# Kernel optimization log

Measured on AMD Instinct MI355X. Metric: run time of the kernel, lower is better.

The kernel has to match this reference:

```python
import jax, jax.numpy as jnp
import numpy as np

D_MODEL = 2048
D_FF = 2048  # must equal D_MODEL: original code computes h @ (A@B).T
RANK = 4
ALPHA = 1.0
SCALE = ALPHA / RANK
B_SZ, SEQ = 4, 4096


def setup_inputs() -> dict:
    key = jax.random.key(0)
    ks = jax.random.split(key, 7)
    s1 = 1.0 / np.sqrt(D_MODEL)
    s2 = 1.0 / np.sqrt(D_FF)
    return {
        "x": jax.random.normal(ks[0], (B_SZ, SEQ, D_MODEL), jnp.float32),
        "W1": jax.random.normal(ks[1], (D_FF, D_MODEL), jnp.float32) * s1,   # torch Linear: (out,in)
        "b1": jax.random.normal(ks[2], (D_FF,), jnp.float32) * 0.01,
        "W2": jax.random.normal(ks[3], (D_MODEL, D_FF), jnp.float32) * s2,
        "b2": jax.random.normal(ks[4], (D_MODEL,), jnp.float32) * 0.01,
        "A": jax.random.normal(ks[5], (D_FF, RANK), jnp.float32) * 0.02,
        "B_lora": jax.random.normal(ks[6], (RANK, D_MODEL), jnp.float32) * 0.02,
    }


def reference(x, W1, b1, W2, b2, A, B_lora):
    # h = act(ffn[0](x)); ffn[1] = GELU
    h = jax.nn.gelu(jnp.einsum('bsd,fd->bsf', x, W1) + b1)   # [B,S,D_FF]
    # out = ffn[2](h)
    out = jnp.einsum('bsf,of->bso', h, W2) + b2              # [B,S,D_MODEL]
    # delta = h @ (A @ B).T * scale  (faithful: materializes (D_FF,D_MODEL) then transposes)
    delta = h @ (A @ B_lora).T * SCALE                       # requires D_FF == D_MODEL
    return out + delta
```

## Files before the change

### kernel.cpp

```cpp
#include <hip/hip_runtime.h>

typedef unsigned short u16;
typedef __attribute__((ext_vector_type(8))) short s16x8;
typedef __attribute__((ext_vector_type(4))) float f32x4;

#define D 2048
#define LORA_SCALE 0.25f

__device__ __forceinline__ u16 f2bf(float f) {
  unsigned u = __float_as_uint(f);
  unsigned r = u + 0x7fffu + ((u >> 16) & 1u);
  return (u16)(r >> 16);
}
__device__ __forceinline__ float bf2f(u16 h) {
  return __uint_as_float(((unsigned)h) << 16);
}

__device__ __forceinline__ void gload_lds16(const u16* g, u16* l) {
  __builtin_amdgcn_global_load_lds((const __attribute__((address_space(1))) void*)g,
                                   (__attribute__((address_space(3))) void*)l,
                                   16, 0, 0);
}

__global__ void split_fp32(const float* __restrict__ in, u16* __restrict__ hi,
                           u16* __restrict__ lo, int n4) {
  int i = blockIdx.x * 256 + threadIdx.x;
  if (i >= n4) return;
  float4 v = ((const float4*)in)[i];
  ushort4 h, l;
  h.x = f2bf(v.x); l.x = f2bf(v.x - bf2f(h.x));
  h.y = f2bf(v.y); l.y = f2bf(v.y - bf2f(h.y));
  h.z = f2bf(v.z); l.z = f2bf(v.z - bf2f(h.z));
  h.w = f2bf(v.w); l.w = f2bf(v.w - bf2f(h.w));
  ((ushort4*)hi)[i] = h;
  ((ushort4*)lo)[i] = l;
}

__global__ void w2eff_split(const float* __restrict__ W2, const float* __restrict__ A,
                            const float* __restrict__ Bl, u16* __restrict__ hi,
                            u16* __restrict__ lo) {
  int idx = blockIdx.x * 256 + threadIdx.x;
  int o = idx >> 9;
  int fq = idx & 511;
  float4 w = ((const float4*)(W2 + o * D))[fq];
  float a0 = A[o * 4 + 0], a1 = A[o * 4 + 1], a2 = A[o * 4 + 2], a3 = A[o * 4 + 3];
  float4 r0 = ((const float4*)(Bl + 0 * D))[fq];
  float4 r1 = ((const float4*)(Bl + 1 * D))[fq];
  float4 r2 = ((const float4*)(Bl + 2 * D))[fq];
  float4 r3 = ((const float4*)(Bl + 3 * D))[fq];
  w.x += LORA_SCALE * (a0 * r0.x + a1 * r1.x + a2 * r2.x + a3 * r3.x);
  w.y += LORA_SCALE * (a0 * r0.y + a1 * r1.y + a2 * r2.y + a3 * r3.y);
  w.z += LORA_SCALE * (a0 * r0.z + a1 * r1.z + a2 * r2.z + a3 * r3.z);
  w.w += LORA_SCALE * (a0 * r0.w + a1 * r1.w + a2 * r2.w + a3 * r3.w);
  ushort4 h, l;
  h.x = f2bf(w.x); l.x = f2bf(w.x - bf2f(h.x));
  h.y = f2bf(w.y); l.y = f2bf(w.y - bf2f(h.y));
  h.z = f2bf(w.z); l.z = f2bf(w.z - bf2f(h.z));
  h.w = f2bf(w.w); l.w = f2bf(w.w - bf2f(h.w));
  ((ushort4*)hi)[idx] = h;
  ((ushort4*)lo)[idx] = l;
}

template <int EPI>
__global__ __launch_bounds__(256, 2) void gemm_bt(
    const u16* __restrict__ Ah, const u16* __restrict__ Al,
    const u16* __restrict__ Bh, const u16* __restrict__ Bl,
    const float* __restrict__ bias,
    u16* __restrict__ Oh, u16* __restrict__ Ol, float* __restrict__ Of) {
  __shared__ u16 lds[2][4][128 * 32];

  const int tid = threadIdx.x;
  const int brow = blockIdx.y * 128;
  const int bcol = blockIdx.x * 128;
  const int lane = tid & 63;
  const int wid = tid >> 6;
  const int wr = (wid >> 1) * 64;
  const int wc = (wid & 1) * 64;
  const int frow = lane & 15;
  const int fk = (lane >> 4) * 8;

  const int s_row = tid >> 2;
  const int s_seg = (tid & 3) * 8;

  auto stage = [&](const u16* __restrict__ G, int rbase, int kt, u16* L) {
    const u16* g = G + (size_t)(rbase + s_row) * D + kt * 32 + s_seg;
    gload_lds16(g, L + tid * 8);
    gload_lds16(g + 64 * D, L + 2048 + tid * 8);
  };

  f32x4 acc[4][4];
#pragma unroll
  for (int i = 0; i < 4; ++i)
#pragma unroll
    for (int j = 0; j < 4; ++j) acc[i][j] = (f32x4){0.f, 0.f, 0.f, 0.f};

  stage(Ah, brow, 0, &lds[0][0][0]);
  stage(Al, brow, 0, &lds[0][1][0]);
  stage(Bh, bcol, 0, &lds[0][2][0]);
  stage(Bl, bcol, 0, &lds[0][3][0]);
  __syncthreads();

  for (int kt = 0; kt < D / 32; ++kt) {
    const int b = kt & 1;
    if (kt < D / 32 - 1) {
      stage(Ah, brow, kt + 1, &lds[b ^ 1][0][0]);
      stage(Al, brow, kt + 1, &lds[b ^ 1][1][0]);
      stage(Bh, bcol, kt + 1, &lds[b ^ 1][2][0]);
      stage(Bl, bcol, kt + 1, &lds[b ^ 1][3][0]);
    }
    s16x8 ah[4], al[4], bh[4], bl[4];
#pragma unroll
    for (int i = 0; i < 4; ++i) {
      const int off = (wr + i * 16 + frow) * 32 + fk;
      ah[i] = *(const s16x8*)&lds[b][0][off];
      al[i] = *(const s16x8*)&lds[b][1][off];
    }
#pragma unroll
    for (int j = 0; j < 4; ++j) {
      const int off = (wc + j * 16 + frow) * 32 + fk;
      bh[j] = *(const s16x8*)&lds[b][2][off];
      bl[j] = *(const s16x8*)&lds[b][3][off];
    }
#pragma unroll
    for (int i = 0; i < 4; ++i)
#pragma unroll
      for (int j = 0; j < 4; ++j) {
        acc[i][j] = __builtin_amdgcn_mfma_f32_16x16x32_bf16(ah[i], bh[j], acc[i][j], 0, 0, 0);
        acc[i][j] = __builtin_amdgcn_mfma_f32_16x16x32_bf16(ah[i], bl[j], acc[i][j], 0, 0, 0);
        acc[i][j] = __builtin_amdgcn_mfma_f32_16x16x32_bf16(al[i], bh[j], acc[i][j], 0, 0, 0);
      }
    __syncthreads();
  }

  const int r0 = brow + wr + (lane >> 4) * 4;
  const int c0 = bcol + wc + (lane & 15);
#pragma unroll
  for (int j = 0; j < 4; ++j) {
    const int col = c0 + j * 16;
    const float bv = bias[col];
#pragma unroll
    for (int i = 0; i < 4; ++i) {
#pragma unroll
      for (int r = 0; r < 4; ++r) {
        const size_t row = r0 + i * 16 + r;
        float v = acc[i][j][r] + bv;
        if (EPI == 0) {
          float t = 0.7978845608028654f * v * (1.0f + 0.044715f * v * v);
          float g = 0.5f * v * (1.0f + tanhf(t));
          u16 hh = f2bf(g);
          u16 hl = f2bf(g - bf2f(hh));
          Oh[row * D + col] = hh;
          Ol[row * D + col] = hl;
        } else {
          Of[row * D + col] = v;
        }
      }
    }
  }
}

extern "C" void kernel_launch(void* const* d_in, const int* in_sizes, int n_in,
                              void* d_out, int out_size, void* d_ws, size_t ws_size,
                              hipStream_t stream) {
  const float* x  = (const float*)d_in[0];
  const float* W1 = (const float*)d_in[1];
  const float* b1 = (const float*)d_in[2];
  const float* W2 = (const float*)d_in[3];
  const float* b2 = (const float*)d_in[4];
  const float* A  = (const float*)d_in[5];
  const float* Bl = (const float*)d_in[6];
  float* out = (float*)d_out;

  char* ws = (char*)d_ws;
  const size_t WBUF = (size_t)D * D * sizeof(u16);
  u16* W1h = (u16*)(ws);
  u16* W1l = (u16*)(ws + WBUF);
  u16* W2h = (u16*)(ws + 2 * WBUF);
  u16* W2l = (u16*)(ws + 3 * WBUF);
  char* cb = ws + 4 * WBUF;

  const int M = 16384;
  int CHUNK = M;
  while (CHUNK > 128 && 4 * WBUF + (size_t)CHUNK * D * 2 * 4 > ws_size) CHUNK >>= 1;

  u16* Xh = (u16*)cb;
  u16* Xl = Xh + (size_t)CHUNK * D;
  u16* Hh = Xl + (size_t)CHUNK * D;
  u16* Hl = Hh + (size_t)CHUNK * D;

  split_fp32<<<dim3((D * D / 4) / 256), 256, 0, stream>>>(W1, W1h, W1l, D * D / 4);
  w2eff_split<<<dim3((D * D / 4) / 256), 256, 0, stream>>>(W2, A, Bl, W2h, W2l);

  for (int c = 0; c < M / CHUNK; ++c) {
    const float* xc = x + (size_t)c * CHUNK * D;
    split_fp32<<<dim3((CHUNK * D / 4) / 256), 256, 0, stream>>>(xc, Xh, Xl, CHUNK * D / 4);
    dim3 grid(D / 128, CHUNK / 128);
    gemm_bt<0><<<grid, 256, 0, stream>>>(Xh, Xl, W1h, W1l, b1, Hh, Hl, nullptr);
    gemm_bt<1><<<grid, 256, 0, stream>>>(Hh, Hl, W2h, W2l, b2, nullptr, nullptr,
                                         out + (size_t)c * CHUNK * D);
  }
}
```

Baseline: 998.8 us.

## Replace GEMM with 256x256 8-wave triple-buffered ping-pong pipeline and XOR-swizzled LDS

Rewrites the split-bf16 GEMM as a 256x256 tile kernel with 8 waves, a 3-stage LDS ring and barrier-separated phases with raised priority around the MFMA groups. The three bf16 cross-products (hi*hi, hi*lo, lo*hi) become a K loop of 192 steps that switches source buffers, rather than three MFMAs per step. It adds an XOR swizzle on LDS reads and writes to avoid bank conflicts, plus a block-index remap for L2 locality. The aim is to overlap global-to-LDS loads with compute and to reuse each operand across more MFMAs. The risks are higher register pressure from 32 accumulators and sensitivity to the correctness of the hand-counted vmcnt waits.

```diff
diff --git a/kernel.cpp b/kernel.cpp
--- a/kernel.cpp
+++ b/kernel.cpp
@@ -62,91 +62,131 @@
 }
 
 template <int EPI>
-__global__ __launch_bounds__(256, 2) void gemm_bt(
+__global__ __launch_bounds__(512, 2) void gemm8p(
     const u16* __restrict__ Ah, const u16* __restrict__ Al,
     const u16* __restrict__ Bh, const u16* __restrict__ Bl,
     const float* __restrict__ bias,
     u16* __restrict__ Oh, u16* __restrict__ Ol, float* __restrict__ Of) {
-  __shared__ u16 lds[2][4][128 * 32];
-
-  const int tid = threadIdx.x;
-  const int brow = blockIdx.y * 128;
-  const int bcol = blockIdx.x * 128;
+  __shared__ u16 lds[3][2][256 * 32];
+
+  const int tid  = threadIdx.x;
   const int lane = tid & 63;
-  const int wid = tid >> 6;
-  const int wr = (wid >> 1) * 64;
-  const int wc = (wid & 1) * 64;
-  const int frow = lane & 15;
-  const int fk = (lane >> 4) * 8;
-
-  const int s_row = tid >> 2;
-  const int s_seg = (tid & 3) * 8;
-
-  auto stage = [&](const u16* __restrict__ G, int rbase, int kt, u16* L) {
-    const u16* g = G + (size_t)(rbase + s_row) * D + kt * 32 + s_seg;
-    gload_lds16(g, L + tid * 8);
-    gload_lds16(g + 64 * D, L + 2048 + tid * 8);
-  };
-
-  f32x4 acc[4][4];
-#pragma unroll
-  for (int i = 0; i < 4; ++i)
+  const int wid  = tid >> 6;
+  const int wrow = wid >> 2;
+  const int wcol = wid & 3;
+
+  const int nwg = gridDim.x;
+  const int cpx = nwg >> 3;
+  const int swz = ((int)blockIdx.x & 7) * cpx + ((int)blockIdx.x >> 3);
+  const int brow = (swz >> 3) * 256;
+  const int bcol = (swz & 7) * 256;
+
+  const int srow  = tid >> 2;
+  const int sslot = (tid & 3) ^ ((tid >> 3) & 3);
+  const int uswz = (((lane >> 4) ^ ((lane & 15) >> 1)) & 3) << 4;
+
+  auto stageA = [&](int t, int rb) {
+    const u16* g = ((t < 128) ? Ah : Al) +
+                   (size_t)(brow + srow) * D + (t & 63) * 32 + sslot * 8;
+    u16* l = &lds[rb][0][0];
+    gload_lds16(g, l + tid * 8);
+    gload_lds16(g + (size_t)128 * D, l + 4096 + tid * 8);
+  };
+  auto stageB = [&](int t, int rb) {
+    const u16* g = ((t < 64) ? Bh : ((t < 128) ? Bl : Bh)) +
+                   (size_t)(bcol + srow) * D + (t & 63) * 32 + sslot * 8;
+    u16* l = &lds[rb][1][0];
+    gload_lds16(g, l + tid * 8);
+    gload_lds16(g + (size_t)128 * D, l + 4096 + tid * 8);
+  };
+  auto rdA = [&](int rb, int r) -> s16x8 {
+    return *(const s16x8*)((const char*)&lds[rb][0][0] + r * 64 + uswz);
+  };
+  auto rdB = [&](int rb, int r) -> s16x8 {
+    return *(const s16x8*)((const char*)&lds[rb][1][0] + r * 64 + uswz);
+  };
+
+  f32x4 acc[8][4];
+#pragma unroll
+  for (int i = 0; i < 8; ++i)
 #pragma unroll
     for (int j = 0; j < 4; ++j) acc[i][j] = (f32x4){0.f, 0.f, 0.f, 0.f};
 
-  stage(Ah, brow, 0, &lds[0][0][0]);
-  stage(Al, brow, 0, &lds[0][1][0]);
-  stage(Bh, bcol, 0, &lds[0][2][0]);
-  stage(Bl, bcol, 0, &lds[0][3][0]);
-  __syncthreads();
-
-  for (int kt = 0; kt < D / 32; ++kt) {
-    const int b = kt & 1;
-    if (kt < D / 32 - 1) {
-      stage(Ah, brow, kt + 1, &lds[b ^ 1][0][0]);
-      stage(Al, brow, kt + 1, &lds[b ^ 1][1][0]);
-      stage(Bh, bcol, kt + 1, &lds[b ^ 1][2][0]);
-      stage(Bl, bcol, kt + 1, &lds[b ^ 1][3][0]);
+  stageA(0, 0); stageB(0, 0);
+  stageA(1, 1); stageB(1, 1);
+  asm volatile("s_waitcnt vmcnt(4)" ::: "memory");
+  __builtin_amdgcn_s_barrier();
+  __builtin_amdgcn_sched_barrier(0);
+
+  const int T = 192;
+  const int l15 = lane & 15;
+  int cur = 0;
+  s16x8 bf[4];
+  for (int t = 0; t < T; ++t) {
+    const int nb = (cur >= 1) ? cur - 1 : cur + 2;
+    const int ts = (t + 2 < T) ? (t + 2) : (T - 1);
+
+    s16x8 af0 = rdA(cur, wrow * 128 + 0 * 16 + l15);
+    s16x8 af1 = rdA(cur, wrow * 128 + 1 * 16 + l15);
+    s16x8 af2 = rdA(cur, wrow * 128 + 2 * 16 + l15);
+    s16x8 af3 = rdA(cur, wrow * 128 + 3 * 16 + l15);
+#pragma unroll
+    for (int j = 0; j < 4; ++j) bf[j] = rdB(cur, wcol * 64 + j * 16 + l15);
+    stageA(ts, nb);
+    __builtin_amdgcn_s_barrier();
+    __builtin_amdgcn_sched_barrier(0);
+    __builtin_amdgcn_s_setprio(1);
+#pragma unroll
+    for (int j = 0; j < 4; ++j) {
+      acc[0][j] = __builtin_amdgcn_mfma_f32_16x16x32_bf16(af0, bf[j], acc[0][j], 0, 0, 0);
+      acc[1][j] = __builtin_amdgcn_mfma_f32_16x16x32_bf16(af1, bf[j], acc[1][j], 0, 0, 0);
+      acc[2][j] = __builtin_amdgcn_mfma_f32_16x16x32_bf16(af2, bf[j], acc[2][j], 0, 0, 0);
+      acc[3][j] = __builtin_amdgcn_mfma_f32_16x16x32_bf16(af3, bf[j], acc[3][j], 0, 0, 0);
     }
-    s16x8 ah[4], al[4], bh[4], bl[4];
-#pragma unroll
-    for (int i = 0; i < 4; ++i) {
-      const int off = (wr + i * 16 + frow) * 32 + fk;
-      ah[i] = *(const s16x8*)&lds[b][0][off];
-      al[i] = *(const s16x8*)&lds[b][1][off];
+    __builtin_amdgcn_s_setprio(0);
+    __builtin_amdgcn_s_barrier();
+    __builtin_amdgcn_sched_barrier(0);
+
+    s16x8 ag0 = rdA(cur, wrow * 128 + 64 + 0 * 16 + l15);
+    s16x8 ag1 = rdA(cur, wrow * 128 + 64 + 1 * 16 + l15);
+    s16x8 ag2 = rdA(cur, wrow * 128 + 64 + 2 * 16 + l15);
+    s16x8 ag3 = rdA(cur, wrow * 128 + 64 + 3 * 16 + l15);
+    stageB(ts, nb);
+    __builtin_amdgcn_s_barrier();
+    __builtin_amdgcn_sched_barrier(0);
+    __builtin_amdgcn_s_setprio(1);
+#pragma unroll
+    for (int j = 0; j < 4; ++j) {
+      acc[4][j] = __builtin_amdgcn_mfma_f32_16x16x32_bf16(ag0, bf[j], acc[4][j], 0, 0, 0);
+      acc[5][j] = __builtin_amdgcn_mfma_f32_16x16x32_bf16(ag1, bf[j], acc[5][j], 0, 0, 0);
+      acc[6][j] = __builtin_amdgcn_mfma_f32_16x16x32_bf16(ag2, bf[j], acc[6][j], 0, 0, 0);
+      acc[7][j] = __builtin_amdgcn_mfma_f32_16x16x32_bf16(ag3, bf[j], acc[7][j], 0, 0, 0);
     }
-#pragma unroll
-    for (int j = 0; j < 4; ++j) {
-      const int off = (wc + j * 16 + frow) * 32 + fk;
-      bh[j] = *(const s16x8*)&lds[b][2][off];
-      bl[j] = *(const s16x8*)&lds[b][3][off];
-    }
-#pragma unroll
-    for (int i = 0; i < 4; ++i)
-#pragma unroll
-      for (int j = 0; j < 4; ++j) {
-        acc[i][j] = __builtin_amdgcn_mfma_f32_16x16x32_bf16(ah[i], bh[j], acc[i][j], 0, 0, 0);
-        acc[i][j] = __builtin_amdgcn_mfma_f32_16x16x32_bf16(ah[i], bl[j], acc[i][j], 0, 0, 0);
-        acc[i][j] = __builtin_amdgcn_mfma_f32_16x16x32_bf16(al[i], bh[j], acc[i][j], 0, 0, 0);
-      }
-    __syncthreads();
+    __builtin_amdgcn_s_setprio(0);
+    asm volatile("s_waitcnt vmcnt(4)" ::: "memory");
+    __builtin_amdgcn_s_barrier();
+    __builtin_amdgcn_sched_barrier(0);
+
+    cur = (cur + 1 >= 3) ? 0 : cur + 1;
   }
 
-  const int r0 = brow + wr + (lane >> 4) * 4;
-  const int c0 = bcol + wc + (lane & 15);
+  asm volatile("s_waitcnt vmcnt(0)" ::: "memory");
+
+  const int r0 = brow + wrow * 128 + (lane >> 4) * 4;
+  const int c0 = bcol + wcol * 64 + l15;
 #pragma unroll
   for (int j = 0; j < 4; ++j) {
     const int col = c0 + j * 16;
     const float bv = bias[col];
 #pragma unroll
-    for (int i = 0; i < 4; ++i) {
+    for (int i = 0; i < 8; ++i) {
 #pragma unroll
       for (int r = 0; r < 4; ++r) {
         const size_t row = r0 + i * 16 + r;
         float v = acc[i][j][r] + bv;
         if (EPI == 0) {
-          float t = 0.7978845608028654f * v * (1.0f + 0.044715f * v * v);
-          float g = 0.5f * v * (1.0f + tanhf(t));
+          float tt = 0.7978845608028654f * v * (1.0f + 0.044715f * v * v);
+          float g = 0.5f * v * (1.0f + tanhf(tt));
           u16 hh = f2bf(g);
           u16 hl = f2bf(g - bf2f(hh));
           Oh[row * D + col] = hh;
@@ -181,7 +221,7 @@
 
   const int M = 16384;
   int CHUNK = M;
-  while (CHUNK > 128 && 4 * WBUF + (size_t)CHUNK * D * 2 * 4 > ws_size) CHUNK >>= 1;
+  while (CHUNK > 256 && 4 * WBUF + (size_t)CHUNK * D * 2 * 4 > ws_size) CHUNK >>= 1;
 
   u16* Xh = (u16*)cb;
   u16* Xl = Xh + (size_t)CHUNK * D;
@@ -194,9 +234,9 @@
   for (int c = 0; c < M / CHUNK; ++c) {
     const float* xc = x + (size_t)c * CHUNK * D;
     split_fp32<<<dim3((CHUNK * D / 4) / 256), 256, 0, stream>>>(xc, Xh, Xl, CHUNK * D / 4);
-    dim3 grid(D / 128, CHUNK / 128);
-    gemm_bt<0><<<grid, 256, 0, stream>>>(Xh, Xl, W1h, W1l, b1, Hh, Hl, nullptr);
-    gemm_bt<1><<<grid, 256, 0, stream>>>(Hh, Hl, W2h, W2l, b2, nullptr, nullptr,
-                                         out + (size_t)c * CHUNK * D);
+    dim3 grid((CHUNK / 256) * (D / 256));
+    gemm8p<0><<<grid, 512, 0, stream>>>(Xh, Xl, W1h, W1l, b1, Hh, Hl, nullptr);
+    gemm8p<1><<<grid, 512, 0, stream>>>(Hh, Hl, W2h, W2l, b2, nullptr, nullptr,
+                                        out + (size_t)c * CHUNK * D);
   }
 }
```

After: 982.3 us. Within noise of the previous version (-1.7%).
